# Kernel optimization log

Measured on AMD Instinct MI355X. Metric: run time of the kernel, lower is better.

## Reference

```python
import jax, jax.numpy as jnp
import numpy as np

N = 50000   # nodes
E = 800000  # edges
D = 256     # num_features == embedding_num
L = 3       # gcn layers
G = 512     # graphs in batch


def setup_inputs() -> dict:
    key = jax.random.key(0)
    ks = jax.random.split(key, 7)
    x = jax.random.normal(ks[0], (N, D), dtype=jnp.float32)
    edge_index = jax.random.randint(ks[1], (2, E), 0, N, dtype=jnp.int32)
    batch = jnp.sort(jax.random.randint(ks[2], (N,), 0, G, dtype=jnp.int32))
    s = 0.05
    Ws1 = jax.random.normal(ks[3], (L, D, D), dtype=jnp.float32) * s
    bs1 = jnp.zeros((L, D), dtype=jnp.float32)
    Ws2 = jax.random.normal(ks[4], (L, D, D), dtype=jnp.float32) * s
    bs2 = jnp.zeros((L, D), dtype=jnp.float32)
    return {"x": x, "edge_index": edge_index, "batch": batch,
            "Ws1": Ws1, "bs1": bs1, "Ws2": Ws2, "bs2": bs2}


def reference(x, edge_index, batch, Ws1, bs1, Ws2, bs2):
    src, dst = edge_index[0], edge_index[1]
    h = x
    xs = []
    for i in range(L):
        # GINConv (eps=0): h_i' = MLP( h_i + sum_{j->i} h_j )
        agg = h + jax.ops.segment_sum(h[src], dst, num_segments=N)  # [N, D]
        t = jnp.maximum(agg @ Ws1[i] + bs1[i], 0.0)                 # inner ReLU
        h = jnp.maximum(t @ Ws2[i] + bs2[i], 0.0)                   # outer F.relu
        xs.append(h)
    # global mean pool per layer output, keyed by graph id
    ones = jnp.ones((N, 1), dtype=x.dtype)
    counts = jnp.clip(jax.ops.segment_sum(ones, batch, num_segments=G), 1.0)  # [G,1]
    pooled = [jax.ops.segment_sum(h_i, batch, num_segments=G) / counts for h_i in xs]
    graph_embed = jnp.concatenate(pooled, axis=1)  # [G, L*D]
    node_embed = jnp.concatenate(xs, axis=1)       # [N, L*D]
    return graph_embed, node_embed
```

## Files before the change

### kernel.cpp

```cpp
#include <hip/hip_runtime.h>

#define NN 50000
#define EE 800000
#define DD 256
#define LL 3
#define GG 512
#define MPAD 50048

typedef __attribute__((ext_vector_type(4))) _Float16 half4;
typedef __attribute__((ext_vector_type(8))) _Float16 half8;
typedef __attribute__((ext_vector_type(16))) float floatx16;

#define CONV_B 12500
#define WPK_B  192
#define HIST_B 3125

__global__ void k_prep(const float* __restrict__ x, _Float16* __restrict__ h16,
                       const float* __restrict__ Ws1, const float* __restrict__ Ws2,
                       _Float16* __restrict__ Wp,
                       const int* __restrict__ dst, int* __restrict__ deg) {
    int b = blockIdx.x;
    if (b < CONV_B) {
        int i = b * 256 + threadIdx.x;
        if (i >= NN * DD / 4) return;
        float4 v = ((const float4*)x)[i];
        half4 o;
        o.x = (_Float16)v.x; o.y = (_Float16)v.y; o.z = (_Float16)v.z; o.w = (_Float16)v.w;
        ((half4*)h16)[i] = o;
    } else if (b < CONV_B + WPK_B) {
        int tid  = (b - CONV_B) * 256 + threadIdx.x;
        int lane = tid & 63;
        int nt   = (tid >> 6) & 7;
        int ks   = (tid >> 9) & 15;
        int w    = tid >> 13;
        if (w >= 6) return;
        int l = w >> 1, s = w & 1;
        const float* W = (s == 0 ? Ws1 : Ws2) + (size_t)l * DD * DD;
        int kbase = ks * 16 + (lane >> 5) * 8;
        int n     = nt * 32 + (lane & 31);
        half8 hi;
#pragma unroll
        for (int j = 0; j < 8; ++j) hi[j] = (_Float16)W[(size_t)(kbase + j) * DD + n];
        ((half8*)Wp)[(((size_t)w * 16 + ks) * 8 + nt) * 64 + lane] = hi;
    } else {
        int i = (b - CONV_B - WPK_B) * 256 + threadIdx.x;
        if (i < EE) atomicAdd(&deg[dst[i]], 1);
    }
}

__global__ void k_scan1(const int* __restrict__ deg, int* __restrict__ rp,
                        int* __restrict__ bsum, int n) {
    __shared__ int s[1024];
    int t = threadIdx.x;
    int i = blockIdx.x * 1024 + t;
    int v = (i < n) ? deg[i] : 0;
    s[t] = v;
    __syncthreads();
    for (int off = 1; off < 1024; off <<= 1) {
        int tmp = (t >= off) ? s[t - off] : 0;
        __syncthreads();
        s[t] += tmp;
        __syncthreads();
    }
    if (i < n) rp[i] = s[t] - v;
    if (t == 1023) bsum[blockIdx.x] = s[1023];
}

__global__ void k_scan2(int* __restrict__ bsum, int nb, int* __restrict__ total_out) {
    int lane = threadIdx.x & 63;
    int v = (lane < nb) ? bsum[lane] : 0;
    int orig = v;
    for (int off = 1; off < 64; off <<= 1) {
        int u = __shfl_up(v, off);
        if (lane >= off) v += u;
    }
    if (lane < nb) bsum[lane] = v - orig;
    if (lane == 63) *total_out = v;
}

__global__ void k_scan3(int* __restrict__ rp, const int* __restrict__ bsum,
                        int* __restrict__ cursor, int n) {
    int i = blockIdx.x * 1024 + threadIdx.x;
    if (i < n) {
        int v = rp[i] + bsum[blockIdx.x];
        rp[i] = v;
        cursor[i] = v;
    }
}

__global__ void k_scatter(const int* __restrict__ src, const int* __restrict__ dst,
                          int* __restrict__ cursor, int* __restrict__ csr_src, int e) {
    int i = blockIdx.x * blockDim.x + threadIdx.x;
    if (i < e) {
        int d = dst[i];
        int pos = atomicAdd(&cursor[d], 1);
        csr_src[pos] = src[i];
    }
}

__global__ __launch_bounds__(256) void k_gather(
        const _Float16* __restrict__ h,
        const int* __restrict__ row_ptr,
        const int* __restrict__ csr_src,
        _Float16* __restrict__ agg) {
    __shared__ int eidx[1024];
    __shared__ int rp_s[5];
    int t = threadIdx.x, lane = t & 63, w = t >> 6;
    int n0 = blockIdx.x * 4;
    if (t < 5) {
        int nn = n0 + t;
        if (nn > NN) nn = NN;
        rp_s[t] = row_ptr[nn];
    }
    __syncthreads();
    int beg0 = rp_s[0];
    int cnt  = rp_s[4] - beg0;
    for (int i = t; i < cnt && i < 1024; i += 256) eidx[i] = csr_src[beg0 + i];
    __syncthreads();

    int n = n0 + w;
    if (n >= NN) return;
    int beg = rp_s[w] - beg0, end = rp_s[w + 1] - beg0;
    int hf = lane >> 5;
    int cl = lane & 31;
    const half8* hp = (const half8*)h;

    half8 acc;
#pragma unroll
    for (int i = 0; i < 8; ++i) acc[i] = (_Float16)0;
    if (hf == 0) acc = hp[(size_t)n * 32 + cl];

    if (cnt <= 1024) {
        int k = beg;
        for (; k + 16 <= end; k += 16) {
            half8 v[8];
#pragma unroll
            for (int u = 0; u < 8; ++u) {
                int s = eidx[k + 2 * u + hf];
                v[u] = hp[(size_t)s * 32 + cl];
            }
#pragma unroll
            for (int u = 0; u < 8; ++u) acc += v[u];
        }
        if (k < end) {
#pragma unroll
            for (int u = 0; u < 8; ++u) {
                int e = k + 2 * u + hf;
                half8 v;
#pragma unroll
                for (int i = 0; i < 8; ++i) v[i] = (_Float16)0;
                if (e < end) v = hp[(size_t)eidx[e] * 32 + cl];
                acc += v;
            }
        }
    } else {
        int k = beg;
        for (; k + 16 <= end; k += 16) {
            half8 v[8];
#pragma unroll
            for (int u = 0; u < 8; ++u) {
                int s = csr_src[beg0 + k + 2 * u + hf];
                v[u] = hp[(size_t)s * 32 + cl];
            }
#pragma unroll
            for (int u = 0; u < 8; ++u) acc += v[u];
        }
        if (k < end) {
#pragma unroll
            for (int u = 0; u < 8; ++u) {
                int e = k + 2 * u + hf;
                half8 v;
#pragma unroll
                for (int i = 0; i < 8; ++i) v[i] = (_Float16)0;
                if (e < end) v = hp[(size_t)csr_src[beg0 + e] * 32 + cl];
                acc += v;
            }
        }
    }

    int4 ai = *(int4*)&acc;
    int4 bi;
    bi.x = __shfl_xor(ai.x, 32);
    bi.y = __shfl_xor(ai.y, 32);
    bi.z = __shfl_xor(ai.z, 32);
    bi.w = __shfl_xor(ai.w, 32);
    acc += *(half8*)&bi;
    if (hf == 0) ((half8*)(agg + (size_t)n * DD))[cl] = acc;
}

__global__ __launch_bounds__(256) void k_mlp(
        const _Float16* __restrict__ A,
        const int* __restrict__ batch,
        const _Float16* __restrict__ Wp1, const float* __restrict__ b1,
        const _Float16* __restrict__ Wp2, const float* __restrict__ b2,
        _Float16* __restrict__ Hout,
        float* __restrict__ Fout,
        float* __restrict__ Gout) {
    __shared__ _Float16 t_lds[64 * 256];
    __shared__ int batch_s[64];
    int t    = threadIdx.x;
    int lane = t & 63;
    int w    = t >> 6;
    int wm   = w >> 1, wn = w & 1;
    int r0   = blockIdx.x * 64;

    if (t < 64) {
        int r = r0 + t;
        batch_s[t] = (r < NN) ? batch[r] : 0x7fffffff;
    }

    int arow = r0 + wm * 32 + (lane & 31);
    const half8* baseA = (const half8*)(A + (size_t)arow * DD) + (lane >> 5);
    const half8* B1    = (const half8*)Wp1;

    floatx16 acc[4];
#pragma unroll
    for (int nt = 0; nt < 4; ++nt)
#pragma unroll
        for (int i = 0; i < 16; ++i) acc[nt][i] = 0.0f;

#pragma unroll 4
    for (int ks = 0; ks < 16; ++ks) {
        half8 a = baseA[ks * 2];
#pragma unroll
        for (int nt = 0; nt < 4; ++nt) {
            half8 b = B1[(size_t)(ks * 8 + wn * 4 + nt) * 64 + lane];
            acc[nt] = __builtin_amdgcn_mfma_f32_32x32x16_f16(a, b, acc[nt], 0, 0, 0);
        }
    }

#pragma unroll
    for (int nt = 0; nt < 4; ++nt) {
        int c  = wn * 128 + nt * 32 + (lane & 31);
        float bv = b1[c];
#pragma unroll
        for (int reg = 0; reg < 16; ++reg) {
            int lr = wm * 32 + (reg & 3) + 8 * (reg >> 2) + 4 * (lane >> 5);
            float v = fmaxf(acc[nt][reg] + bv, 0.0f);
            t_lds[lr * 256 + ((((c >> 3) ^ (lr & 7)) << 3) | (c & 7))] = (_Float16)v;
        }
    }
    __syncthreads();

    const half8* B2 = (const half8*)Wp2;
    int r = wm * 32 + (lane & 31);
    floatx16 acc2[4];
#pragma unroll
    for (int nt = 0; nt < 4; ++nt)
#pragma unroll
        for (int i = 0; i < 16; ++i) acc2[nt][i] = 0.0f;

#pragma unroll 4
    for (int ks = 0; ks < 16; ++ks) {
        int kblk = ks * 2 + (lane >> 5);
        half8 a = *(const half8*)&t_lds[r * 256 + ((kblk ^ (r & 7)) << 3)];
#pragma unroll
        for (int nt = 0; nt < 4; ++nt) {
            half8 b = B2[(size_t)(ks * 8 + wn * 4 + nt) * 64 + lane];
            acc2[nt] = __builtin_amdgcn_mfma_f32_32x32x16_f16(a, b, acc2[nt], 0, 0, 0);
        }
    }

    const int rbase = wm * 32 + 4 * (lane >> 5);
#pragma unroll
    for (int nt = 0; nt < 4; ++nt) {
        int col = wn * 128 + nt * 32 + (lane & 31);
        float bv = b2[col];
#pragma unroll
        for (int reg = 0; reg < 16; ++reg) {
            int rowid = rbase + (reg & 3) + 8 * (reg >> 2);
            int row = r0 + rowid;
            if (row < NN) {
                float v = fmaxf(acc2[nt][reg] + bv, 0.0f);
                Hout[(size_t)row * DD + col] = (_Float16)v;
                __builtin_nontemporal_store(v, &Fout[(size_t)row * 768 + col]);
            }
        }
    }

    int lastid = NN - 1 - r0 - wm * 32;
    if (lastid >= 0) {
        if (lastid > 31) lastid = 31;
        int g0 = batch_s[wm * 32];
        int g1 = batch_s[wm * 32 + lastid];
        for (int g = g0; g <= g1; ++g) {
#pragma unroll
            for (int nt = 0; nt < 4; ++nt) {
                int col = wn * 128 + nt * 32 + (lane & 31);
                float bv = b2[col];
                float s = 0.0f;
#pragma unroll
                for (int reg = 0; reg < 16; ++reg) {
                    int rowid = rbase + (reg & 3) + 8 * (reg >> 2);
                    if (batch_s[rowid] == g)
                        s += fmaxf(acc2[nt][reg] + bv, 0.0f);
                }
                s += __shfl_xor(s, 32);
                if (lane < 32)
                    atomicAdd(&Gout[(size_t)g * 768 + col], s);
            }
        }
    }
}

__global__ void k_pool_final(const float* __restrict__ gsum,
                             const int* __restrict__ batch,
                             float* __restrict__ graph_embed) {
    int g = blockIdx.x;
    int t = threadIdx.x;
    int start, end;
    { int l = 0, h = NN; while (l < h) { int m = (l + h) >> 1; if (batch[m] < g) l = m + 1; else h = m; } start = l; }
    { int l = 0, h = NN; while (l < h) { int m = (l + h) >> 1; if (batch[m] < g + 1) l = m + 1; else h = m; } end = l; }
    int cnt = end - start;
    float inv = 1.0f / (float)(cnt > 0 ? cnt : 1);
    float4 v = ((const float4*)(gsum + (size_t)g * 768))[t];
    float4 o; o.x = v.x * inv; o.y = v.y * inv; o.z = v.z * inv; o.w = v.w * inv;
    ((float4*)(graph_embed + (size_t)g * 768))[t] = o;
}

extern "C" void kernel_launch(void* const* d_in, const int* in_sizes, int n_in,
                              void* d_out, int out_size, void* d_ws, size_t ws_size,
                              hipStream_t stream) {
    const float* x     = (const float*)d_in[0];
    const int*   ei    = (const int*)d_in[1];
    const int*   batch = (const int*)d_in[2];
    const float* Ws1   = (const float*)d_in[3];
    const float* bs1   = (const float*)d_in[4];
    const float* Ws2   = (const float*)d_in[5];
    const float* bs2   = (const float*)d_in[6];

    float* out         = (float*)d_out;
    float* graph_embed = out;
    float* node_embed  = out + (size_t)GG * 768;

    _Float16* h16   = (_Float16*)d_ws;
    _Float16* agg16 = h16 + (size_t)MPAD * DD;
    _Float16* Wp    = agg16 + (size_t)MPAD * DD;
    float* gsum     = (float*)(Wp + (size_t)6 * 65536);
    int* cursor     = (int*)(gsum + (size_t)GG * 768);
    int* bsum       = cursor + NN;
    int* csr_src    = bsum + 64;
    int* row_ptr    = csr_src + EE;

    const int* src = ei;
    const int* dst = ei + EE;

    const int NB = (NN + 1023) / 1024;

    hipMemsetAsync(gsum, 0, (size_t)GG * 768 * 4 + (size_t)NN * 4 + 64 * 4, stream);

    k_prep<<<CONV_B + WPK_B + HIST_B, 256, 0, stream>>>(x, h16, Ws1, Ws2, Wp, dst, cursor);

    k_scan1<<<NB, 1024, 0, stream>>>(cursor, row_ptr, bsum, NN);
    k_scan2<<<1, 64, 0, stream>>>(bsum, NB, row_ptr + NN);
    k_scan3<<<NB, 1024, 0, stream>>>(row_ptr, bsum, cursor, NN);
    k_scatter<<<(EE + 255) / 256, 256, 0, stream>>>(src, dst, cursor, csr_src, EE);

    for (int l = 0; l < LL; ++l) {
        k_gather<<<(NN + 3) / 4, 256, 0, stream>>>(h16, row_ptr, csr_src, agg16);
        k_mlp<<<MPAD / 64, 256, 0, stream>>>(
            agg16, batch,
            Wp + (size_t)(2 * l + 0) * 65536, bs1 + (size_t)l * DD,
            Wp + (size_t)(2 * l + 1) * 65536, bs2 + (size_t)l * DD,
            h16, node_embed + (size_t)l * DD, gsum + (size_t)l * DD);
    }

    k_pool_final<<<GG, 192, 0, stream>>>(gsum, batch, graph_embed);
}
```

Baseline: 618.7 us.

## Fuse gather and MLP into one per-layer kernel with flag-based tile handoff

Merges the neighbour gather and the two-GEMM MLP into a single launch per layer. Each 64-row tile gets 16 gather blocks and one MLP block. The MLP block spins on a per-tile atomic counter until its 16 gather blocks have written agg, so gather and MLP work can overlap across tiles and the per-layer launch gap goes away. Because the MLP now runs concurrently with gathers that still read h, the node features are double-buffered across layers. This relies on producer blocks being scheduled before or alongside their waiting consumer; because the consumer has the highest block index in its group this should normally hold, but spinning blocks still occupy compute slots.

```diff
diff --git a/kernel.cpp b/kernel.cpp
--- a/kernel.cpp
+++ b/kernel.cpp
@@ -6,6 +6,7 @@
 #define LL 3
 #define GG 512
 #define MPAD 50048
+#define TILES 782
 
 typedef __attribute__((ext_vector_type(4))) _Float16 half4;
 typedef __attribute__((ext_vector_type(8))) _Float16 half8;
@@ -98,119 +99,134 @@
     }
 }
 
-__global__ __launch_bounds__(256) void k_gather(
+__global__ __launch_bounds__(256) void k_layer(
         const _Float16* __restrict__ h,
         const int* __restrict__ row_ptr,
         const int* __restrict__ csr_src,
-        _Float16* __restrict__ agg) {
-    __shared__ int eidx[1024];
-    __shared__ int rp_s[5];
-    int t = threadIdx.x, lane = t & 63, w = t >> 6;
-    int n0 = blockIdx.x * 4;
-    if (t < 5) {
-        int nn = n0 + t;
-        if (nn > NN) nn = NN;
-        rp_s[t] = row_ptr[nn];
-    }
-    __syncthreads();
-    int beg0 = rp_s[0];
-    int cnt  = rp_s[4] - beg0;
-    for (int i = t; i < cnt && i < 1024; i += 256) eidx[i] = csr_src[beg0 + i];
-    __syncthreads();
-
-    int n = n0 + w;
-    if (n >= NN) return;
-    int beg = rp_s[w] - beg0, end = rp_s[w + 1] - beg0;
-    int hf = lane >> 5;
-    int cl = lane & 31;
-    const half8* hp = (const half8*)h;
-
-    half8 acc;
-#pragma unroll
-    for (int i = 0; i < 8; ++i) acc[i] = (_Float16)0;
-    if (hf == 0) acc = hp[(size_t)n * 32 + cl];
-
-    if (cnt <= 1024) {
-        int k = beg;
-        for (; k + 16 <= end; k += 16) {
-            half8 v[8];
-#pragma unroll
-            for (int u = 0; u < 8; ++u) {
-                int s = eidx[k + 2 * u + hf];
-                v[u] = hp[(size_t)s * 32 + cl];
-            }
-#pragma unroll
-            for (int u = 0; u < 8; ++u) acc += v[u];
-        }
-        if (k < end) {
-#pragma unroll
-            for (int u = 0; u < 8; ++u) {
-                int e = k + 2 * u + hf;
-                half8 v;
-#pragma unroll
-                for (int i = 0; i < 8; ++i) v[i] = (_Float16)0;
-                if (e < end) v = hp[(size_t)eidx[e] * 32 + cl];
-                acc += v;
-            }
-        }
-    } else {
-        int k = beg;
-        for (; k + 16 <= end; k += 16) {
-            half8 v[8];
-#pragma unroll
-            for (int u = 0; u < 8; ++u) {
-                int s = csr_src[beg0 + k + 2 * u + hf];
-                v[u] = hp[(size_t)s * 32 + cl];
-            }
-#pragma unroll
-            for (int u = 0; u < 8; ++u) acc += v[u];
-        }
-        if (k < end) {
-#pragma unroll
-            for (int u = 0; u < 8; ++u) {
-                int e = k + 2 * u + hf;
-                half8 v;
-#pragma unroll
-                for (int i = 0; i < 8; ++i) v[i] = (_Float16)0;
-                if (e < end) v = hp[(size_t)csr_src[beg0 + e] * 32 + cl];
-                acc += v;
-            }
-        }
-    }
-
-    int4 ai = *(int4*)&acc;
-    int4 bi;
-    bi.x = __shfl_xor(ai.x, 32);
-    bi.y = __shfl_xor(ai.y, 32);
-    bi.z = __shfl_xor(ai.z, 32);
-    bi.w = __shfl_xor(ai.w, 32);
-    acc += *(half8*)&bi;
-    if (hf == 0) ((half8*)(agg + (size_t)n * DD))[cl] = acc;
-}
-
-__global__ __launch_bounds__(256) void k_mlp(
-        const _Float16* __restrict__ A,
         const int* __restrict__ batch,
         const _Float16* __restrict__ Wp1, const float* __restrict__ b1,
         const _Float16* __restrict__ Wp2, const float* __restrict__ b2,
+        _Float16* __restrict__ agg,
         _Float16* __restrict__ Hout,
         float* __restrict__ Fout,
-        float* __restrict__ Gout) {
+        float* __restrict__ Gout,
+        int* __restrict__ flags) {
     __shared__ _Float16 t_lds[64 * 256];
-    __shared__ int batch_s[64];
     int t    = threadIdx.x;
     int lane = t & 63;
     int w    = t >> 6;
-    int wm   = w >> 1, wn = w & 1;
-    int r0   = blockIdx.x * 64;
-
-    if (t < 64) {
-        int r = r0 + t;
-        batch_s[t] = (r < NN) ? batch[r] : 0x7fffffff;
-    }
+    int grp  = blockIdx.x / 17;
+    int sub  = blockIdx.x % 17;
+
+    if (sub < 16) {
+        int* eidx = (int*)t_lds;
+        int* rp_s = eidx + 1024;
+        int n0 = grp * 64 + sub * 4;
+        if (t < 5) {
+            int nn = n0 + t;
+            if (nn > NN) nn = NN;
+            rp_s[t] = row_ptr[nn];
+        }
+        __syncthreads();
+        int beg0 = rp_s[0];
+        int cnt  = rp_s[4] - beg0;
+        for (int i = t; i < cnt && i < 1024; i += 256) eidx[i] = csr_src[beg0 + i];
+        __syncthreads();
+
+        int n = n0 + w;
+        if (n < NN) {
+            int beg = rp_s[w] - beg0, end = rp_s[w + 1] - beg0;
+            int hf = lane >> 5;
+            int cl = lane & 31;
+            const half8* hp = (const half8*)h;
+
+            half8 acc;
+#pragma unroll
+            for (int i = 0; i < 8; ++i) acc[i] = (_Float16)0;
+            if (hf == 0) acc = hp[(size_t)n * 32 + cl];
+
+            if (cnt <= 1024) {
+                int k = beg;
+                for (; k + 16 <= end; k += 16) {
+                    half8 v[8];
+#pragma unroll
+                    for (int u = 0; u < 8; ++u) {
+                        int s = eidx[k + 2 * u + hf];
+                        v[u] = hp[(size_t)s * 32 + cl];
+                    }
+#pragma unroll
+                    for (int u = 0; u < 8; ++u) acc += v[u];
+                }
+                if (k < end) {
+#pragma unroll
+                    for (int u = 0; u < 8; ++u) {
+                        int e = k + 2 * u + hf;
+                        half8 v;
+#pragma unroll
+                        for (int i = 0; i < 8; ++i) v[i] = (_Float16)0;
+                        if (e < end) v = hp[(size_t)eidx[e] * 32 + cl];
+                        acc += v;
+                    }
+                }
+            } else {
+                int k = beg;
+                for (; k + 16 <= end; k += 16) {
+                    half8 v[8];
+#pragma unroll
+                    for (int u = 0; u < 8; ++u) {
+                        int s = csr_src[beg0 + k + 2 * u + hf];
+                        v[u] = hp[(size_t)s * 32 + cl];
+                    }
+#pragma unroll
+                    for (int u = 0; u < 8; ++u) acc += v[u];
+                }
+                if (k < end) {
+#pragma unroll
+                    for (int u = 0; u < 8; ++u) {
+                        int e = k + 2 * u + hf;
+                        half8 v;
+#pragma unroll
+                        for (int i = 0; i < 8; ++i) v[i] = (_Float16)0;
+                        if (e < end) v = hp[(size_t)csr_src[beg0 + e] * 32 + cl];
+                        acc += v;
+                    }
+                }
+            }
+
+            int4 ai = *(int4*)&acc;
+            int4 bi;
+            bi.x = __shfl_xor(ai.x, 32);
+            bi.y = __shfl_xor(ai.y, 32);
+            bi.z = __shfl_xor(ai.z, 32);
+            bi.w = __shfl_xor(ai.w, 32);
+            acc += *(half8*)&bi;
+            if (hf == 0) {
+                unsigned long long uu[2];
+                __builtin_memcpy(uu, &acc, 16);
+                unsigned long long* p =
+                    (unsigned long long*)(agg + (size_t)n * DD) + (size_t)cl * 2;
+                __hip_atomic_store(p,     uu[0], __ATOMIC_RELAXED, __HIP_MEMORY_SCOPE_AGENT);
+                __hip_atomic_store(p + 1, uu[1], __ATOMIC_RELAXED, __HIP_MEMORY_SCOPE_AGENT);
+            }
+        }
+        __syncthreads();
+        if (t == 0)
+            __hip_atomic_fetch_add(&flags[grp], 1, __ATOMIC_RELAXED, __HIP_MEMORY_SCOPE_AGENT);
+        return;
+    }
+
+    if (t == 0) {
+        while (__hip_atomic_load(&flags[grp], __ATOMIC_RELAXED, __HIP_MEMORY_SCOPE_AGENT) < 16)
+            __builtin_amdgcn_s_sleep(2);
+    }
+    __syncthreads();
+    (void)__hip_atomic_load(&flags[grp], __ATOMIC_ACQUIRE, __HIP_MEMORY_SCOPE_AGENT);
+
+    int wm = (w >> 1) & 1, wn = w & 1;
+    int r0 = grp * 64;
 
     int arow = r0 + wm * 32 + (lane & 31);
-    const half8* baseA = (const half8*)(A + (size_t)arow * DD) + (lane >> 5);
+    const half8* baseA = (const half8*)(agg + (size_t)arow * DD) + (lane >> 5);
     const half8* B1    = (const half8*)Wp1;
 
     floatx16 acc[4];
@@ -260,6 +276,14 @@
             acc2[nt] = __builtin_amdgcn_mfma_f32_32x32x16_f16(a, b, acc2[nt], 0, 0, 0);
         }
     }
+
+    __syncthreads();
+    int* bs = (int*)t_lds;
+    if (t < 64) {
+        int row = r0 + t;
+        bs[t] = (row < NN) ? batch[row] : 0x7fffffff;
+    }
+    __syncthreads();
 
     const int rbase = wm * 32 + 4 * (lane >> 5);
 #pragma unroll
@@ -281,8 +305,8 @@
     int lastid = NN - 1 - r0 - wm * 32;
     if (lastid >= 0) {
         if (lastid > 31) lastid = 31;
-        int g0 = batch_s[wm * 32];
-        int g1 = batch_s[wm * 32 + lastid];
+        int g0 = bs[wm * 32];
+        int g1 = bs[wm * 32 + lastid];
         for (int g = g0; g <= g1; ++g) {
 #pragma unroll
             for (int nt = 0; nt < 4; ++nt) {
@@ -292,7 +316,7 @@
 #pragma unroll
                 for (int reg = 0; reg < 16; ++reg) {
                     int rowid = rbase + (reg & 3) + 8 * (reg >> 2);
-                    if (batch_s[rowid] == g)
+                    if (bs[rowid] == g)
                         s += fmaxf(acc2[nt][reg] + bv, 0.0f);
                 }
                 s += __shfl_xor(s, 32);
@@ -334,10 +358,12 @@
     float* node_embed  = out + (size_t)GG * 768;
 
     _Float16* h16   = (_Float16*)d_ws;
-    _Float16* agg16 = h16 + (size_t)MPAD * DD;
+    _Float16* h_alt = h16 + (size_t)MPAD * DD;
+    _Float16* agg16 = h_alt + (size_t)MPAD * DD;
     _Float16* Wp    = agg16 + (size_t)MPAD * DD;
     float* gsum     = (float*)(Wp + (size_t)6 * 65536);
-    int* cursor     = (int*)(gsum + (size_t)GG * 768);
+    int* flags      = (int*)(gsum + (size_t)GG * 768);
+    int* cursor     = flags + 3 * TILES;
     int* bsum       = cursor + NN;
     int* csr_src    = bsum + 64;
     int* row_ptr    = csr_src + EE;
@@ -347,7 +373,9 @@
 
     const int NB = (NN + 1023) / 1024;
 
-    hipMemsetAsync(gsum, 0, (size_t)GG * 768 * 4 + (size_t)NN * 4 + 64 * 4, stream);
+    hipMemsetAsync(gsum, 0,
+                   (size_t)GG * 768 * 4 + (size_t)3 * TILES * 4 +
+                   (size_t)NN * 4 + 64 * 4, stream);
 
     k_prep<<<CONV_B + WPK_B + HIST_B, 256, 0, stream>>>(x, h16, Ws1, Ws2, Wp, dst, cursor);
 
@@ -357,12 +385,14 @@
     k_scatter<<<(EE + 255) / 256, 256, 0, stream>>>(src, dst, cursor, csr_src, EE);
 
     for (int l = 0; l < LL; ++l) {
-        k_gather<<<(NN + 3) / 4, 256, 0, stream>>>(h16, row_ptr, csr_src, agg16);
-        k_mlp<<<MPAD / 64, 256, 0, stream>>>(
-            agg16, batch,
+        const _Float16* hin  = (l & 1) ? h_alt : h16;
+        _Float16*       hout = (l & 1) ? h16 : h_alt;
+        k_layer<<<TILES * 17, 256, 0, stream>>>(
+            hin, row_ptr, csr_src, batch,
             Wp + (size_t)(2 * l + 0) * 65536, bs1 + (size_t)l * DD,
             Wp + (size_t)(2 * l + 1) * 65536, bs2 + (size_t)l * DD,
-            h16, node_embed + (size_t)l * DD, gsum + (size_t)l * DD);
+            agg16, hout, node_embed + (size_t)l * DD, gsum + (size_t)l * DD,
+            flags + (size_t)l * TILES);
     }
 
     k_pool_final<<<GG, 192, 0, stream>>>(gsum, batch, graph_embed);
```

After: 1.473 ms. 2.38x slower.

## Shard fp16 node features by column groups for cache-local gather

Applied to the files above, without the earlier changes.

Stores h16 and agg16 in a column-sharded layout (8 shards of 32 halves per node, padded to MPAD rows), so each gather block reads only one 64-byte column slice per neighbour. The aim is to keep each shard's working set (about 3.2MB) resident in L2 while blocks with the same shard run together. The gather drops the LDS edge-index staging and gives 16 edge slots per wave, each with 4 parts, followed by a shuffle reduction. The MLP reads and writes the sharded layout with nontemporal accesses and skips writing h16 on the last layer. The cost is 8x more gather blocks, each re-reading row_ptr and csr_src, plus a longer shuffle reduction.

```diff
diff --git a/kernel.cpp b/kernel.cpp
--- a/kernel.cpp
+++ b/kernel.cpp
@@ -6,10 +6,13 @@
 #define LL 3
 #define GG 512
 #define MPAD 50048
+#define NSH 8
 
 typedef __attribute__((ext_vector_type(4))) _Float16 half4;
 typedef __attribute__((ext_vector_type(8))) _Float16 half8;
 typedef __attribute__((ext_vector_type(16))) float floatx16;
+typedef __attribute__((ext_vector_type(4))) int int4v;
+
 
 #define CONV_B 12500
 #define WPK_B  192
@@ -22,11 +25,13 @@
     int b = blockIdx.x;
     if (b < CONV_B) {
         int i = b * 256 + threadIdx.x;
-        if (i >= NN * DD / 4) return;
+        if (i >= NN * 64) return;
         float4 v = ((const float4*)x)[i];
         half4 o;
         o.x = (_Float16)v.x; o.y = (_Float16)v.y; o.z = (_Float16)v.z; o.w = (_Float16)v.w;
-        ((half4*)h16)[i] = o;
+        int r = i >> 6, c4g = i & 63;
+        int shard = c4g >> 3, within = c4g & 7;
+        ((half4*)h16)[((size_t)shard * MPAD + r) * 8 + within] = o;
     } else if (b < CONV_B + WPK_B) {
         int tid  = (b - CONV_B) * 256 + threadIdx.x;
         int lane = tid & 63;
@@ -103,89 +108,48 @@
         const int* __restrict__ row_ptr,
         const int* __restrict__ csr_src,
         _Float16* __restrict__ agg) {
-    __shared__ int eidx[1024];
-    __shared__ int rp_s[5];
     int t = threadIdx.x, lane = t & 63, w = t >> 6;
-    int n0 = blockIdx.x * 4;
-    if (t < 5) {
-        int nn = n0 + t;
-        if (nn > NN) nn = NN;
-        rp_s[t] = row_ptr[nn];
-    }
-    __syncthreads();
-    int beg0 = rp_s[0];
-    int cnt  = rp_s[4] - beg0;
-    for (int i = t; i < cnt && i < 1024; i += 256) eidx[i] = csr_src[beg0 + i];
-    __syncthreads();
-
-    int n = n0 + w;
+    int shard = blockIdx.x & 7;
+    int n = (blockIdx.x >> 3) * 4 + w;
     if (n >= NN) return;
-    int beg = rp_s[w] - beg0, end = rp_s[w + 1] - beg0;
-    int hf = lane >> 5;
-    int cl = lane & 31;
-    const half8* hp = (const half8*)h;
+    int beg = row_ptr[n], end = row_ptr[n + 1];
+    int slot = lane >> 2, part = lane & 3;
+    const half8* hp8 = (const half8*)h;
+    size_t sbase = (size_t)shard * MPAD;
 
     half8 acc;
 #pragma unroll
     for (int i = 0; i < 8; ++i) acc[i] = (_Float16)0;
-    if (hf == 0) acc = hp[(size_t)n * 32 + cl];
-
-    if (cnt <= 1024) {
-        int k = beg;
-        for (; k + 16 <= end; k += 16) {
-            half8 v[8];
-#pragma unroll
-            for (int u = 0; u < 8; ++u) {
-                int s = eidx[k + 2 * u + hf];
-                v[u] = hp[(size_t)s * 32 + cl];
-            }
-#pragma unroll
-            for (int u = 0; u < 8; ++u) acc += v[u];
-        }
-        if (k < end) {
-#pragma unroll
-            for (int u = 0; u < 8; ++u) {
-                int e = k + 2 * u + hf;
-                half8 v;
-#pragma unroll
-                for (int i = 0; i < 8; ++i) v[i] = (_Float16)0;
-                if (e < end) v = hp[(size_t)eidx[e] * 32 + cl];
-                acc += v;
-            }
-        }
-    } else {
-        int k = beg;
-        for (; k + 16 <= end; k += 16) {
-            half8 v[8];
-#pragma unroll
-            for (int u = 0; u < 8; ++u) {
-                int s = csr_src[beg0 + k + 2 * u + hf];
-                v[u] = hp[(size_t)s * 32 + cl];
-            }
-#pragma unroll
-            for (int u = 0; u < 8; ++u) acc += v[u];
-        }
-        if (k < end) {
-#pragma unroll
-            for (int u = 0; u < 8; ++u) {
-                int e = k + 2 * u + hf;
-                half8 v;
-#pragma unroll
-                for (int i = 0; i < 8; ++i) v[i] = (_Float16)0;
-                if (e < end) v = hp[(size_t)csr_src[beg0 + e] * 32 + cl];
-                acc += v;
-            }
-        }
-    }
-
-    int4 ai = *(int4*)&acc;
-    int4 bi;
-    bi.x = __shfl_xor(ai.x, 32);
-    bi.y = __shfl_xor(ai.y, 32);
-    bi.z = __shfl_xor(ai.z, 32);
-    bi.w = __shfl_xor(ai.w, 32);
-    acc += *(half8*)&bi;
-    if (hf == 0) ((half8*)(agg + (size_t)n * DD))[cl] = acc;
+    if (slot == 0) acc = hp8[(sbase + n) * 4 + part];
+
+    for (int k = beg; k < end; k += 32) {
+        int e0 = k + slot, e1 = k + 16 + slot;
+        half8 v0, v1;
+#pragma unroll
+        for (int i = 0; i < 8; ++i) { v0[i] = (_Float16)0; v1[i] = (_Float16)0; }
+        if (e0 < end) {
+            int s = __builtin_nontemporal_load(&csr_src[e0]);
+            v0 = hp8[(sbase + s) * 4 + part];
+        }
+        if (e1 < end) {
+            int s = __builtin_nontemporal_load(&csr_src[e1]);
+            v1 = hp8[(sbase + s) * 4 + part];
+        }
+        acc += v0; acc += v1;
+    }
+
+#pragma unroll
+    for (int m = 4; m < 64; m <<= 1) {
+        int4v a = *(int4v*)&acc, b;
+        b[0] = __shfl_xor(a[0], m);
+        b[1] = __shfl_xor(a[1], m);
+        b[2] = __shfl_xor(a[2], m);
+        b[3] = __shfl_xor(a[3], m);
+        acc += *(half8*)&b;
+    }
+    if (slot == 0)
+        __builtin_nontemporal_store(*(int4v*)&acc,
+                                    (int4v*)agg + (sbase + n) * 4 + part);
 }
 
 __global__ __launch_bounds__(256) void k_mlp(
@@ -209,9 +173,10 @@
         batch_s[t] = (r < NN) ? batch[r] : 0x7fffffff;
     }
 
+    int hf   = lane >> 5;
     int arow = r0 + wm * 32 + (lane & 31);
-    const half8* baseA = (const half8*)(A + (size_t)arow * DD) + (lane >> 5);
-    const half8* B1    = (const half8*)Wp1;
+    const half8* Ash = (const half8*)A;
+    const half8* B1  = (const half8*)Wp1;
 
     floatx16 acc[4];
 #pragma unroll
@@ -221,7 +186,9 @@
 
 #pragma unroll 4
     for (int ks = 0; ks < 16; ++ks) {
-        half8 a = baseA[ks * 2];
+        int cb = ks * 2 + hf;
+        half8 a = __builtin_nontemporal_load(
+            &Ash[((size_t)(cb >> 2) * MPAD + arow) * 4 + (cb & 3)]);
 #pragma unroll
         for (int nt = 0; nt < 4; ++nt) {
             half8 b = B1[(size_t)(ks * 8 + wn * 4 + nt) * 64 + lane];
@@ -266,13 +233,17 @@
     for (int nt = 0; nt < 4; ++nt) {
         int col = wn * 128 + nt * 32 + (lane & 31);
         float bv = b2[col];
+        int shard = wn * 4 + nt;
 #pragma unroll
         for (int reg = 0; reg < 16; ++reg) {
             int rowid = rbase + (reg & 3) + 8 * (reg >> 2);
             int row = r0 + rowid;
             if (row < NN) {
                 float v = fmaxf(acc2[nt][reg] + bv, 0.0f);
-                Hout[(size_t)row * DD + col] = (_Float16)v;
+                if (Hout)
+                    __builtin_nontemporal_store(
+                        (_Float16)v,
+                        &Hout[((size_t)shard * MPAD + row) * 32 + (lane & 31)]);
                 __builtin_nontemporal_store(v, &Fout[(size_t)row * 768 + col]);
             }
         }
@@ -357,12 +328,13 @@
     k_scatter<<<(EE + 255) / 256, 256, 0, stream>>>(src, dst, cursor, csr_src, EE);
 
     for (int l = 0; l < LL; ++l) {
-        k_gather<<<(NN + 3) / 4, 256, 0, stream>>>(h16, row_ptr, csr_src, agg16);
+        k_gather<<<12500 * NSH, 256, 0, stream>>>(h16, row_ptr, csr_src, agg16);
         k_mlp<<<MPAD / 64, 256, 0, stream>>>(
             agg16, batch,
             Wp + (size_t)(2 * l + 0) * 65536, bs1 + (size_t)l * DD,
             Wp + (size_t)(2 * l + 1) * 65536, bs2 + (size_t)l * DD,
-            h16, node_embed + (size_t)l * DD, gsum + (size_t)l * DD);
+            (l == LL - 1) ? nullptr : h16,
+            node_embed + (size_t)l * DD, gsum + (size_t)l * DD);
     }
 
     k_pool_final<<<GG, 192, 0, stream>>>(gsum, batch, graph_embed);
```

Measured after the change: 809.2 us. 1.31x slower.

## Shrink MLP row tile to 32 rows and skip the final-layer fp16 writeback

Applied to the files above, without the earlier changes.

The fused MLP kernel now handles 32 rows per block instead of 64. Each of the four waves covers a 64-column slice of all 32 rows rather than a 32x128 quadrant, which halves the accumulator registers and LDS per block and doubles the number of blocks to improve occupancy and load balance. The cost is that each block re-reads the full weight matrices for half as many rows, roughly doubling weight traffic from L2. The last layer also stops writing the fp16 hidden state, since no later layer reads it.

```diff
diff --git a/kernel.cpp b/kernel.cpp
--- a/kernel.cpp
+++ b/kernel.cpp
@@ -30,18 +30,18 @@
     } else if (b < CONV_B + WPK_B) {
         int tid  = (b - CONV_B) * 256 + threadIdx.x;
         int lane = tid & 63;
-        int nt   = (tid >> 6) & 7;
+        int nb   = (tid >> 6) & 7;
         int ks   = (tid >> 9) & 15;
         int w    = tid >> 13;
         if (w >= 6) return;
         int l = w >> 1, s = w & 1;
         const float* W = (s == 0 ? Ws1 : Ws2) + (size_t)l * DD * DD;
         int kbase = ks * 16 + (lane >> 5) * 8;
-        int n     = nt * 32 + (lane & 31);
+        int n     = nb * 32 + (lane & 31);
         half8 hi;
 #pragma unroll
         for (int j = 0; j < 8; ++j) hi[j] = (_Float16)W[(size_t)(kbase + j) * DD + n];
-        ((half8*)Wp)[(((size_t)w * 16 + ks) * 8 + nt) * 64 + lane] = hi;
+        ((half8*)Wp)[(((size_t)w * 16 + ks) * 8 + nb) * 64 + lane] = hi;
     } else {
         int i = (b - CONV_B - WPK_B) * 256 + threadIdx.x;
         if (i < EE) atomicAdd(&deg[dst[i]], 1);
@@ -196,26 +196,25 @@
         _Float16* __restrict__ Hout,
         float* __restrict__ Fout,
         float* __restrict__ Gout) {
-    __shared__ _Float16 t_lds[64 * 256];
-    __shared__ int batch_s[64];
+    __shared__ _Float16 t_lds[32 * 256];
+    __shared__ int batch_s[32];
     int t    = threadIdx.x;
     int lane = t & 63;
     int w    = t >> 6;
-    int wm   = w >> 1, wn = w & 1;
-    int r0   = blockIdx.x * 64;
-
-    if (t < 64) {
+    int r0   = blockIdx.x * 32;
+
+    if (t < 32) {
         int r = r0 + t;
         batch_s[t] = (r < NN) ? batch[r] : 0x7fffffff;
     }
 
-    int arow = r0 + wm * 32 + (lane & 31);
+    int arow = r0 + (lane & 31);
     const half8* baseA = (const half8*)(A + (size_t)arow * DD) + (lane >> 5);
     const half8* B1    = (const half8*)Wp1;
 
-    floatx16 acc[4];
-#pragma unroll
-    for (int nt = 0; nt < 4; ++nt)
+    floatx16 acc[2];
+#pragma unroll
+    for (int nt = 0; nt < 2; ++nt)
 #pragma unroll
         for (int i = 0; i < 16; ++i) acc[nt][i] = 0.0f;
 
@@ -223,19 +222,19 @@
     for (int ks = 0; ks < 16; ++ks) {
         half8 a = baseA[ks * 2];
 #pragma unroll
-        for (int nt = 0; nt < 4; ++nt) {
-            half8 b = B1[(size_t)(ks * 8 + wn * 4 + nt) * 64 + lane];
+        for (int nt = 0; nt < 2; ++nt) {
+            half8 b = B1[(size_t)(ks * 8 + w * 2 + nt) * 64 + lane];
             acc[nt] = __builtin_amdgcn_mfma_f32_32x32x16_f16(a, b, acc[nt], 0, 0, 0);
         }
     }
 
 #pragma unroll
-    for (int nt = 0; nt < 4; ++nt) {
-        int c  = wn * 128 + nt * 32 + (lane & 31);
+    for (int nt = 0; nt < 2; ++nt) {
+        int c  = w * 64 + nt * 32 + (lane & 31);
         float bv = b1[c];
 #pragma unroll
         for (int reg = 0; reg < 16; ++reg) {
-            int lr = wm * 32 + (reg & 3) + 8 * (reg >> 2) + 4 * (lane >> 5);
+            int lr = (reg & 3) + 8 * (reg >> 2) + 4 * (lane >> 5);
             float v = fmaxf(acc[nt][reg] + bv, 0.0f);
             t_lds[lr * 256 + ((((c >> 3) ^ (lr & 7)) << 3) | (c & 7))] = (_Float16)v;
         }
@@ -243,10 +242,10 @@
     __syncthreads();
 
     const half8* B2 = (const half8*)Wp2;
-    int r = wm * 32 + (lane & 31);
-    floatx16 acc2[4];
-#pragma unroll
-    for (int nt = 0; nt < 4; ++nt)
+    int r = lane & 31;
+    floatx16 acc2[2];
+#pragma unroll
+    for (int nt = 0; nt < 2; ++nt)
 #pragma unroll
         for (int i = 0; i < 16; ++i) acc2[nt][i] = 0.0f;
 
@@ -255,16 +254,16 @@
         int kblk = ks * 2 + (lane >> 5);
         half8 a = *(const half8*)&t_lds[r * 256 + ((kblk ^ (r & 7)) << 3)];
 #pragma unroll
-        for (int nt = 0; nt < 4; ++nt) {
-            half8 b = B2[(size_t)(ks * 8 + wn * 4 + nt) * 64 + lane];
+        for (int nt = 0; nt < 2; ++nt) {
+            half8 b = B2[(size_t)(ks * 8 + w * 2 + nt) * 64 + lane];
             acc2[nt] = __builtin_amdgcn_mfma_f32_32x32x16_f16(a, b, acc2[nt], 0, 0, 0);
         }
     }
 
-    const int rbase = wm * 32 + 4 * (lane >> 5);
-#pragma unroll
-    for (int nt = 0; nt < 4; ++nt) {
-        int col = wn * 128 + nt * 32 + (lane & 31);
+    const int rbase = 4 * (lane >> 5);
+#pragma unroll
+    for (int nt = 0; nt < 2; ++nt) {
+        int col = w * 64 + nt * 32 + (lane & 31);
         float bv = b2[col];
 #pragma unroll
         for (int reg = 0; reg < 16; ++reg) {
@@ -272,21 +271,21 @@
             int row = r0 + rowid;
             if (row < NN) {
                 float v = fmaxf(acc2[nt][reg] + bv, 0.0f);
-                Hout[(size_t)row * DD + col] = (_Float16)v;
+                if (Hout) Hout[(size_t)row * DD + col] = (_Float16)v;
                 __builtin_nontemporal_store(v, &Fout[(size_t)row * 768 + col]);
             }
         }
     }
 
-    int lastid = NN - 1 - r0 - wm * 32;
+    int lastid = NN - 1 - r0;
     if (lastid >= 0) {
         if (lastid > 31) lastid = 31;
-        int g0 = batch_s[wm * 32];
-        int g1 = batch_s[wm * 32 + lastid];
+        int g0 = batch_s[0];
+        int g1 = batch_s[lastid];
         for (int g = g0; g <= g1; ++g) {
 #pragma unroll
-            for (int nt = 0; nt < 4; ++nt) {
-                int col = wn * 128 + nt * 32 + (lane & 31);
+            for (int nt = 0; nt < 2; ++nt) {
+                int col = w * 64 + nt * 32 + (lane & 31);
                 float bv = b2[col];
                 float s = 0.0f;
 #pragma unroll
@@ -358,11 +357,12 @@
 
     for (int l = 0; l < LL; ++l) {
         k_gather<<<(NN + 3) / 4, 256, 0, stream>>>(h16, row_ptr, csr_src, agg16);
-        k_mlp<<<MPAD / 64, 256, 0, stream>>>(
+        k_mlp<<<MPAD / 32, 256, 0, stream>>>(
             agg16, batch,
             Wp + (size_t)(2 * l + 0) * 65536, bs1 + (size_t)l * DD,
             Wp + (size_t)(2 * l + 1) * 65536, bs2 + (size_t)l * DD,
-            h16, node_embed + (size_t)l * DD, gsum + (size_t)l * DD);
+            (l == LL - 1) ? nullptr : h16,
+            node_embed + (size_t)l * DD, gsum + (size_t)l * DD);
     }
 
     k_pool_final<<<GG, 192, 0, stream>>>(gsum, batch, graph_embed);
```

Result: faster. 594.8 us (-3.9%).
